# Performance work log

Hardware: AMD Instinct MI355X
Metric: run time of the kernel (lower is better)

Reference implementation:

```python
import jax, jax.numpy as jnp
import numpy as np

B, C, H, W, R = 8, 256, 64, 64, 16


def setup_inputs() -> dict:
    key = jax.random.key(0)
    ks = jax.random.split(key, 14)
    def w(k, shape, fan):
        return (jax.random.normal(k, shape, jnp.float32) / np.sqrt(fan)).astype(jnp.float32)
    return {
        "features_depth": jax.random.normal(ks[0], (B, C, H, W), jnp.float32),
        "features_semseg": jax.random.normal(ks[1], (B, C, H, W), jnp.float32),
        "W0": w(ks[2], (C, 2 * C), 2 * C),          # conv_split0 1x1, [out,in]
        "Wdw": w(ks[3], (C, 1, 3, 3), 9),            # depthwise 3x3, groups=C
        "Wq": w(ks[4], (C, C), C),                   # Linear weights [out,in]
        "Wk": w(ks[5], (C, C), C),
        "Wv": w(ks[6], (C, C), C),
        "Wp": w(ks[7], (C, C), C),
        "bp": jnp.zeros((C,), jnp.float32),
        "Wsplit": w(ks[8], (C, C), C),               # conv_split 1x1
        "se_d_w1": w(ks[9], (C // R, C), C),         # SE squeeze conv1x1 (depth)
        "se_d_w2": w(ks[10], (C, C // R), C // R),
        "se_s_w1": w(ks[11], (C // R, C), C),        # SE squeeze conv1x1 (semseg)
        "se_s_w2": w(ks[12], (C, C // R), C // R),
    }


def _l2norm(a, eps=1e-12):
    n = jnp.linalg.norm(a, axis=-1, keepdims=True)
    return a / jnp.maximum(n, eps)


def _se(x, w1, w2):
    # x: [B,C,H,W]; global avg pool -> 1x1 convs -> sigmoid gate
    p = x.mean(axis=(2, 3))                                  # [B,C]
    h = jax.nn.relu(jnp.einsum('rc,bc->br', w1, p))          # [B,C/R]
    g = jax.nn.sigmoid(jnp.einsum('cr,br->bc', w2, h))       # [B,C]
    return x * g[:, :, None, None]


def reference(features_depth, features_semseg, W0, Wdw, Wq, Wk, Wv, Wp, bp,
              Wsplit, se_d_w1, se_d_w2, se_s_w1, se_s_w2):
    x = jnp.concatenate([features_depth, features_semseg], axis=1)  # [B,2C,H,W]
    x = jnp.einsum('oc,bchw->bohw', W0, x)                          # 1x1 conv
    x = jax.lax.conv_general_dilated(
        x, Wdw, window_strides=(1, 1), padding='SAME',
        dimension_numbers=('NCHW', 'OIHW', 'NCHW'), feature_group_count=C)
    xt = x.transpose(0, 2, 3, 1).reshape(B, H * W, C)               # [B,N,C]
    q = (xt @ Wq.T).transpose(0, 2, 1)                              # [B,C,N]
    k = (xt @ Wk.T).transpose(0, 2, 1)
    v = (xt @ Wv.T).transpose(0, 2, 1)
    q = _l2norm(q)
    k = _l2norm(k)
    attn = jax.nn.softmax(jnp.einsum('bcn,bdn->bcd', k, q), axis=-1)  # [B,C,C]
    y = jnp.einsum('bcd,bdn->bcn', attn, v)                         # [B,C,N]
    y = y.transpose(0, 2, 1)                                        # [B,N,C]
    y = y @ Wp.T + bp                                               # proj
    out_c = y.reshape(B, H, W, C).transpose(0, 3, 1, 2)             # [B,C,H,W]
    out_c = jnp.einsum('oc,bchw->bohw', Wsplit, out_c)              # 1x1 conv
    out_depth = _se(out_c, se_d_w1, se_d_w2) + features_depth
    out_semseg = _se(out_c, se_s_w1, se_s_w2) + features_semseg
    return (out_depth, out_semseg)
```

## Files before the change

kernel.cpp:

```cpp
#include <hip/hip_runtime.h>
#include <cstdint>

#define DEVI __device__ __forceinline__

using fx4 = __attribute__((ext_vector_type(4))) float;
using bf8 = __attribute__((ext_vector_type(8))) __bf16;
using s8v = __attribute__((ext_vector_type(8))) short;
using s4v = __attribute__((ext_vector_type(4))) short;
typedef unsigned short u16;
typedef unsigned int u32;

DEVI float b2f(u16 u) { return __builtin_bit_cast(float, (u32)u << 16); }
DEVI u16 f2b(float f) {
  u32 u = __builtin_bit_cast(u32, f);
  return (u16)((u + 0x7fffu + ((u >> 16) & 1u)) >> 16);
}

#define GLOAD(g, l)                                                          \
  __builtin_amdgcn_global_load_lds(                                          \
      (const __attribute__((address_space(1))) unsigned int*)(g),            \
      (__attribute__((address_space(3))) unsigned int*)(l), 16, 0, 0)

__global__ __launch_bounds__(256) void prep(const float* __restrict__ W0,
                                            const float* __restrict__ Wq,
                                            const float* __restrict__ Wk,
                                            const float* __restrict__ Wv,
                                            u16* __restrict__ w0b,
                                            u16* __restrict__ wqk2,
                                            u16* __restrict__ wvtb) {
  const int i = blockIdx.x * 256 + threadIdx.x;
  if (blockIdx.y == 0) {
    if (i < 131072) w0b[i] = f2b(W0[i]);
  } else if (blockIdx.y == 1) {
    if (i < 524288) {
      const int row = i >> 9, c = i & 511;
      const float* src = (row < 256) ? Wq : Wk;
      wqk2[i] = f2b(src[((row & 255) << 8) + (c & 255)]);
    }
  } else {
    if (i < 65536) {
      const int e = i >> 8, d = i & 255;
      wvtb[i] = f2b(Wv[d * 256 + e]);
    }
  }
}

__global__ __launch_bounds__(256) void wcmul(const float* __restrict__ Wsp,
                                             const float* __restrict__ Wp,
                                             const float* __restrict__ bp,
                                             u16* __restrict__ wcb, float* __restrict__ bc) {
  const int o = blockIdx.x, t = threadIdx.x;
  __shared__ float row[256];
  __shared__ float red[4];
  row[t] = Wsp[o * 256 + t];
  __syncthreads();
  float acc = 0.f;
  for (int c = 0; c < 256; ++c) acc += row[c] * Wp[c * 256 + t];
  wcb[o * 256 + t] = f2b(acc);
  float pb = row[t] * bp[t];
#pragma unroll
  for (int m = 32; m > 0; m >>= 1) pb += __shfl_xor(pb, m);
  if ((t & 63) == 0) red[t >> 6] = pb;
  __syncthreads();
  if (t == 0) bc[o] = red[0] + red[1] + red[2] + red[3];
}

__global__ void pack_cat(const float* __restrict__ fd, const float* __restrict__ fs,
                         u16* __restrict__ out) {
  __shared__ float t[32][33];
  const int b = blockIdx.z;
  const int n0 = blockIdx.x * 32;
  const int g = blockIdx.y;
  const float* src = (g < 8) ? fd : fs;
  const int c0 = (g & 7) * 32;
  const int ccol0 = g * 32;
  const int tx = threadIdx.x;
  const int ty = threadIdx.y;
  const float* sp = src + ((long)b * 256 + c0) * 4096 + n0;
#pragma unroll
  for (int i = 0; i < 4; ++i) {
    int c = ty + i * 8;
    t[c][tx] = sp[(long)c * 4096 + tx];
  }
  __syncthreads();
  u16* op = out + ((long)b * 4096 + n0) * 512 + ccol0;
#pragma unroll
  for (int i = 0; i < 4; ++i) {
    int r = ty + i * 8;
    op[(long)r * 512 + tx] = f2b(t[tx][r]);
  }
}

template <typename OT, int BIAS, bool POOL, int EPI>
__global__ __launch_bounds__(256) void gemm_nt(
    const u16* __restrict__ A, long sA, int lda,
    const u16* __restrict__ B, long sB, int ldb,
    OT* __restrict__ C, long sC, long sCs, int ldc,
    const float* __restrict__ bias, int Keff, int ksplit,
    float* __restrict__ poolpart,
    const float* __restrict__ wqf, const float* __restrict__ wkf,
    float* __restrict__ dpart) {
  __shared__ u16 ldsA[128 * 64];
  __shared__ u16 ldsB[128 * 64];
  const int z = blockIdx.z;
  const int bb = z / ksplit;
  const int ss = z - bb * ksplit;
  const int bm = blockIdx.x * 128;
  const int bn = blockIdx.y * 128;
  const u16* Ab = A + bb * sA + (long)ss * Keff + (long)bm * lda;
  const u16* Bb = B + bb * sB + (long)ss * Keff + (long)bn * ldb;
  const int tid = threadIdx.x;
  const int wid = tid >> 6;
  const int lane = tid & 63;
  const int wm = wid >> 1, wn = wid & 1;
  const int srow = tid >> 3;
  const int slot = tid & 7;

  fx4 acc[4][4] = {};
  for (int kt = 0; kt < Keff; kt += 64) {
#pragma unroll
    for (int i = 0; i < 4; ++i) {
      const int row = i * 32 + srow;
      const int kq = slot ^ (row & 7);
      GLOAD(Ab + (long)row * lda + kt + kq * 8, &ldsA[i * 2048 + wid * 512]);
      GLOAD(Bb + (long)row * ldb + kt + kq * 8, &ldsB[i * 2048 + wid * 512]);
    }
    __syncthreads();
#pragma unroll
    for (int ko = 0; ko < 2; ++ko) {
      bf8 af[4], bfr[4];
      const int kq = ko * 4 + (lane >> 4);
#pragma unroll
      for (int f = 0; f < 4; ++f) {
        const int ar = wm * 64 + f * 16 + (lane & 15);
        af[f] = *(const bf8*)&ldsA[ar * 64 + ((kq ^ (ar & 7)) * 8)];
        const int br = wn * 64 + f * 16 + (lane & 15);
        bfr[f] = *(const bf8*)&ldsB[br * 64 + ((kq ^ (br & 7)) * 8)];
      }
#pragma unroll
      for (int fm = 0; fm < 4; ++fm)
#pragma unroll
        for (int fn = 0; fn < 4; ++fn)
          acc[fm][fn] = __builtin_amdgcn_mfma_f32_16x16x32_bf16(af[fm], bfr[fn], acc[fm][fn], 0, 0, 0);
    }
    __syncthreads();
  }
  if constexpr (EPI == 1) {
    u16* S2b = (u16*)C + bb * sC;
    float dp[4][4];
#pragma unroll
    for (int fm = 0; fm < 4; ++fm)
#pragma unroll
      for (int r = 0; r < 4; ++r) dp[fm][r] = 0.f;
#pragma unroll
    for (int fm = 0; fm < 4; ++fm) {
      const int m0 = bm + wm * 64 + fm * 16 + ((lane >> 4) << 2);
#pragma unroll
      for (int fn = 0; fn < 4; ++fn) {
        const int n0 = bn + wn * 64 + fn * 16 + (lane & 15);
#pragma unroll
        for (int r = 0; r < 4; ++r) {
          const float v = acc[fm][fn][r];
          const int m = m0 + r;
          if (m < 256) {
            const u16 hi = f2b(v);
            S2b[(long)m * 512 + n0] = hi;
            S2b[(long)m * 512 + 256 + n0] = f2b(v - b2f(hi));
          }
          const float* wr = (m < 256) ? (wqf + (long)m * 256) : (wkf + (long)(m - 256) * 256);
          dp[fm][r] += v * wr[n0];
        }
      }
    }
#pragma unroll
    for (int fm = 0; fm < 4; ++fm)
#pragma unroll
      for (int r = 0; r < 4; ++r) {
        float s = dp[fm][r];
        s += __shfl_xor(s, 1); s += __shfl_xor(s, 2);
        s += __shfl_xor(s, 4); s += __shfl_xor(s, 8);
        if ((lane & 15) == 0) {
          const int m = bm + wm * 64 + fm * 16 + ((lane >> 4) << 2) + r;
          dpart[(long)(blockIdx.y * 2 + wn) * 4096 + bb * 512 + m] = s;
        }
      }
    return;
  }
  OT* Cb = C + bb * sC + ss * sCs;
  float pr[4][4];
  if (POOL) {
#pragma unroll
    for (int fm = 0; fm < 4; ++fm)
#pragma unroll
      for (int r = 0; r < 4; ++r) pr[fm][r] = 0.f;
  }
#pragma unroll
  for (int fm = 0; fm < 4; ++fm) {
    const int m0 = bm + wm * 64 + fm * 16 + ((lane >> 4) << 2);
#pragma unroll
    for (int fn = 0; fn < 4; ++fn) {
      const int n0 = bn + wn * 64 + fn * 16 + (lane & 15);
#pragma unroll
      for (int r = 0; r < 4; ++r) {
        float v = acc[fm][fn][r];
        if (BIAS == 2) v += bias[m0 + r];
        if constexpr (sizeof(OT) == 2) Cb[(long)(m0 + r) * ldc + n0] = (OT)f2b(v);
        else Cb[(long)(m0 + r) * ldc + n0] = v;
        if (POOL) pr[fm][r] += v;
      }
    }
  }
  if (POOL) {
#pragma unroll
    for (int fm = 0; fm < 4; ++fm)
#pragma unroll
      for (int r = 0; r < 4; ++r) {
        float s = pr[fm][r];
        s += __shfl_xor(s, 1); s += __shfl_xor(s, 2);
        s += __shfl_xor(s, 4); s += __shfl_xor(s, 8);
        if ((lane & 15) == 0) {
          const int o = bm + wm * 64 + fm * 16 + ((lane >> 4) << 2) + r;
          poolpart[(long)(blockIdx.y * 2 + wn) * 2048 + bb * 256 + o] = s;
        }
      }
  }
}

__global__ __launch_bounds__(256) void dwconv3x3(const u16* __restrict__ x,
                                                 const float* __restrict__ wdw,
                                                 u16* __restrict__ y) {
  __shared__ float w[9][256];
  const int t = threadIdx.x;
  for (int i = t; i < 2304; i += 256) w[i % 9][i / 9] = wdw[i];
  __syncthreads();
  const int nb = blockIdx.x;
  const int b = nb >> 9;
  const int n0 = (nb & 511) << 3;
  const int tn = t >> 5;
  const int tc = (t & 31) << 3;
  const int n = n0 + tn;
  const int hh = n >> 6, ww2 = n & 63;
  const u16* base = x + ((long)b << 20);
  float acc[8] = {0.f, 0.f, 0.f, 0.f, 0.f, 0.f, 0.f, 0.f};
#pragma unroll
  for (int ky = 0; ky < 3; ++ky) {
    const int hy = hh + ky - 1;
    if ((unsigned)hy >= 64u) continue;
#pragma unroll
    for (int kx = 0; kx < 3; ++kx) {
      const int wx = ww2 + kx - 1;
      if ((unsigned)wx >= 64u) continue;
      const s8v v = *(const s8v*)&base[(((hy << 6) + wx) << 8) + tc];
      const int kk = ky * 3 + kx;
      const fx4 wa = *(const fx4*)&w[kk][tc];
      const fx4 wb = *(const fx4*)&w[kk][tc + 4];
#pragma unroll
      for (int j = 0; j < 4; ++j) {
        acc[j] += wa[j] * b2f((u16)v[j]);
        acc[4 + j] += wb[j] * b2f((u16)v[4 + j]);
      }
    }
  }
  s8v o;
#pragma unroll
  for (int j = 0; j < 8; ++j) o[j] = (short)f2b(acc[j]);
  *(s8v*)&y[((long)b << 20) + ((long)n << 8) + tc] = o;
}

__global__ void btrans(const u16* __restrict__ x, u16* __restrict__ y) {
  __shared__ u16 t[32][34];
  const int b = blockIdx.z;
  const int n0 = blockIdx.x * 32;
  const int c0 = blockIdx.y * 32;
  const int tx = threadIdx.x, ty = threadIdx.y;
  const u16* sp = x + (long)b * 1048576 + (long)n0 * 256 + c0;
#pragma unroll
  for (int j = 0; j < 4; ++j) {
    int i = ty + j * 8;
    t[i][tx] = sp[(long)i * 256 + tx];
  }
  __syncthreads();
  u16* op = y + (long)b * 1048576 + (long)c0 * 4096 + n0;
#pragma unroll
  for (int j = 0; j < 4; ++j) {
    int r = ty + j * 8;
    op[(long)r * 4096 + tx] = t[tx][r];
  }
}

__global__ __launch_bounds__(256) void gsplit(const float* __restrict__ part,
                                              u16* __restrict__ G2) {
  const int i4 = (blockIdx.x * 256 + threadIdx.x) * 4;
  fx4 s = {0.f, 0.f, 0.f, 0.f};
#pragma unroll
  for (int ss = 0; ss < 8; ++ss) s += *(const fx4*)(part + (long)ss * 524288 + i4);
  const int b = i4 >> 16, rem = i4 & 65535, e = rem >> 8, c0 = rem & 255;
  u16* d = G2 + (long)b * 131072 + (long)e * 512 + c0;
  s4v hi, lo;
#pragma unroll
  for (int j = 0; j < 4; ++j) {
    u16 h = f2b(s[j]);
    hi[j] = (short)h;
    lo[j] = (short)f2b(s[j] - b2f(h));
  }
  *(s4v*)d = hi;
  *(s4v*)(d + 256) = lo;
}

__global__ __launch_bounds__(256) void softmax_g2(const float* __restrict__ araw,
                                                  const float* __restrict__ dpart,
                                                  u16* __restrict__ out) {
  const int wid = threadIdx.x >> 6, lane = threadIdx.x & 63;
  const int t = threadIdx.x;
  const int b = blockIdx.x >> 6;
  __shared__ float rq[256];
  float dq = dpart[b * 512 + t] + dpart[4096 + b * 512 + t] +
             dpart[8192 + b * 512 + t] + dpart[12288 + b * 512 + t];
  rq[t] = 1.f / fmaxf(sqrtf(fmaxf(dq, 0.f)), 1e-12f);
  __syncthreads();
  const long row = (long)blockIdx.x * 4 + wid;
  const int c = (int)(row & 255);
  const int ki = b * 512 + 256 + c;
  float dk = dpart[ki] + dpart[4096 + ki] + dpart[8192 + ki] + dpart[12288 + ki];
  const float rk = 1.f / fmaxf(sqrtf(fmaxf(dk, 0.f)), 1e-12f);
  fx4 v = ((const fx4*)(araw + row * 256))[lane];
  v[0] *= rk * rq[lane * 4];     v[1] *= rk * rq[lane * 4 + 1];
  v[2] *= rk * rq[lane * 4 + 2]; v[3] *= rk * rq[lane * 4 + 3];
  float m = fmaxf(fmaxf(v[0], v[1]), fmaxf(v[2], v[3]));
#pragma unroll
  for (int o = 32; o > 0; o >>= 1) m = fmaxf(m, __shfl_xor(m, o));
  float e0 = __expf(v[0] - m), e1 = __expf(v[1] - m);
  float e2 = __expf(v[2] - m), e3 = __expf(v[3] - m);
  float s4 = e0 + e1 + e2 + e3;
#pragma unroll
  for (int o = 32; o > 0; o >>= 1) s4 += __shfl_xor(s4, o);
  const float inv = 1.f / s4;
  u16* op = out + row * 256 + lane * 4;
  op[0] = f2b(e0 * inv); op[1] = f2b(e1 * inv);
  op[2] = f2b(e2 * inv); op[3] = f2b(e3 * inv);
}

__global__ __launch_bounds__(256) void se_gates(const float* __restrict__ poolpart,
                                                const float* __restrict__ w1d, const float* __restrict__ w2d,
                                                const float* __restrict__ w1s, const float* __restrict__ w2s,
                                                float* __restrict__ gd, float* __restrict__ gs) {
  const int b = blockIdx.x;
  const int t = threadIdx.x;
  __shared__ float p[256], hd[16], hs[16];
  float s = 0.f;
#pragma unroll 8
  for (int sl = 0; sl < 64; ++sl) s += poolpart[(long)sl * 2048 + b * 256 + t];
  p[t] = s * (1.f / 4096.f);
  __syncthreads();
  if (t < 16) {
    float ad = 0.f, as2 = 0.f;
    for (int j = 0; j < 256; ++j) {
      ad += w1d[t * 256 + j] * p[j];
      as2 += w1s[t * 256 + j] * p[j];
    }
    hd[t] = fmaxf(ad, 0.f);
    hs[t] = fmaxf(as2, 0.f);
  }
  __syncthreads();
  float ad = 0.f, as2 = 0.f;
#pragma unroll
  for (int r = 0; r < 16; ++r) {
    ad += w2d[t * 16 + r] * hd[r];
    as2 += w2s[t * 16 + r] * hs[r];
  }
  gd[b * 256 + t] = 1.f / (1.f + __expf(-ad));
  gs[b * 256 + t] = 1.f / (1.f + __expf(-as2));
}

__global__ __launch_bounds__(256) void fuse_out2(const u16* __restrict__ oc,
                                                 const u16* __restrict__ cat,
                                                 const float* __restrict__ gd,
                                                 const float* __restrict__ gs,
                                                 float* __restrict__ od,
                                                 float* __restrict__ os) {
  __shared__ u16 td[32][68];
  __shared__ u16 ts2[32][68];
  const int b = blockIdx.z;
  const int c0 = blockIdx.y * 32;
  const int n0 = blockIdx.x * 64;
  const int t = threadIdx.x;
  {
    const int n = t >> 2, cj = (t & 3) * 8;
    const u16* cb = cat + ((long)b * 4096 + n0 + n) * 512 + c0 + cj;
    const s8v vd = *(const s8v*)cb;
    const s8v vs = *(const s8v*)(cb + 256);
#pragma unroll
    for (int j = 0; j < 8; ++j) {
      td[cj + j][n] = (u16)vd[j];
      ts2[cj + j][n] = (u16)vs[j];
    }
  }
  __syncthreads();
  const int c = t >> 3, no = (t & 7) * 8;
  const long obase = ((long)b * 256 + c0 + c) * 4096 + n0 + no;
  const float gdv = gd[b * 256 + c0 + c];
  const float gsv = gs[b * 256 + c0 + c];
  const s8v o8 = *(const s8v*)&oc[obase];
  fx4 r0, r1, q0, q1;
#pragma unroll
  for (int j = 0; j < 4; ++j) {
    const float vl = b2f((u16)o8[j]);
    const float vh = b2f((u16)o8[4 + j]);
    r0[j] = vl * gdv + b2f(td[c][no + j]);
    r1[j] = vh * gdv + b2f(td[c][no + 4 + j]);
    q0[j] = vl * gsv + b2f(ts2[c][no + j]);
    q1[j] = vh * gsv + b2f(ts2[c][no + 4 + j]);
  }
  *(fx4*)(od + obase) = r0; *(fx4*)(od + obase + 4) = r1;
  *(fx4*)(os + obase) = q0; *(fx4*)(os + obase + 4) = q1;
}

extern "C" void kernel_launch(void* const* d_in, const int* in_sizes, int n_in,
                              void* d_out, int out_size, void* d_ws, size_t ws_size,
                              hipStream_t stream) {
  const float* fd  = (const float*)d_in[0];
  const float* fs  = (const float*)d_in[1];
  const float* W0  = (const float*)d_in[2];
  const float* Wdw = (const float*)d_in[3];
  const float* Wq  = (const float*)d_in[4];
  const float* Wk  = (const float*)d_in[5];
  const float* Wv  = (const float*)d_in[6];
  const float* Wp  = (const float*)d_in[7];
  const float* bp  = (const float*)d_in[8];
  const float* Wsp = (const float*)d_in[9];
  const float* w1d = (const float*)d_in[10];
  const float* w2d = (const float*)d_in[11];
  const float* w1s = (const float*)d_in[12];
  const float* w2s = (const float*)d_in[13];

  char* ws = (char*)d_ws;
  u16* catb   = (u16*)(ws + 0);
  u16* x0b    = (u16*)(ws + 33554432);
  u16* outcb  = x0b;
  u16* xtb    = (u16*)(ws + 50331648);
  u16* xtT    = (u16*)(ws + 67108864);
  float* part = (float*)(ws + 83886080);
  u16* G2     = (u16*)(ws + 100663296);
  u16* S2     = (u16*)(ws + 102760448);
  float* araw = (float*)(ws + 104857600);
  u16* attnb  = (u16*)(ws + 106954752);
  u16* m1t    = (u16*)(ws + 108003328);
  u16* wfin   = (u16*)(ws + 109051904);
  u16* w0b    = (u16*)(ws + 110100480);
  u16* wqk2   = (u16*)(ws + 110362624);
  u16* wvtb   = (u16*)(ws + 110886912);
  u16* wcb    = (u16*)(ws + 111017984);
  float* bcb  = (float*)(ws + 111149056);
  float* dpart = (float*)(ws + 111150080);
  float* poolpart = (float*)(ws + 111215616);
  float* gdp  = (float*)(ws + 111739904);
  float* gsp  = (float*)(ws + 111748096);
  float* od  = (float*)d_out;
  float* osg = od + 8388608;

  prep<<<dim3(2048, 3), 256, 0, stream>>>(W0, Wq, Wk, Wv, w0b, wqk2, wvtb);
  wcmul<<<256, 256, 0, stream>>>(Wsp, Wp, bp, wcb, bcb);
  pack_cat<<<dim3(128, 16, 8), dim3(32, 8), 0, stream>>>(fd, fs, catb);
  gemm_nt<u16, 0, false, 0><<<dim3(32, 2, 8), 256, 0, stream>>>(
      catb, 2097152, 512, w0b, 0, 512, x0b, 1048576, 0, 256, nullptr, 512, 1,
      nullptr, nullptr, nullptr, nullptr);
  dwconv3x3<<<4096, 256, 0, stream>>>(x0b, Wdw, xtb);
  btrans<<<dim3(128, 8, 8), dim3(32, 8), 0, stream>>>(xtb, xtT);
  gemm_nt<float, 0, false, 0><<<dim3(2, 2, 64), 256, 0, stream>>>(
      xtT, 1048576, 4096, xtT, 1048576, 4096,
      part, 65536, 524288, 256, nullptr, 512, 8, nullptr, nullptr, nullptr, nullptr);
  gsplit<<<512, 256, 0, stream>>>(part, G2);
  gemm_nt<u16, 0, false, 1><<<dim3(4, 2, 8), 256, 0, stream>>>(
      wqk2, 0, 512, G2, 131072, 512, S2, 131072, 0, 512, nullptr, 512, 1,
      nullptr, Wq, Wk, dpart);
  gemm_nt<float, 0, false, 0><<<dim3(2, 2, 8), 256, 0, stream>>>(
      wqk2 + 131072, 0, 512, S2, 131072, 512, araw, 65536, 0, 256, nullptr, 512, 1,
      nullptr, nullptr, nullptr, nullptr);
  softmax_g2<<<512, 256, 0, stream>>>(araw, dpart, attnb);
  gemm_nt<u16, 0, false, 0><<<dim3(2, 2, 8), 256, 0, stream>>>(
      wvtb, 0, 256, attnb, 65536, 256, m1t, 65536, 0, 256, nullptr, 256, 1,
      nullptr, nullptr, nullptr, nullptr);
  gemm_nt<u16, 0, false, 0><<<dim3(2, 2, 8), 256, 0, stream>>>(
      wcb, 0, 256, m1t, 65536, 256, wfin, 65536, 0, 256, nullptr, 256, 1,
      nullptr, nullptr, nullptr, nullptr);
  gemm_nt<u16, 2, true, 0><<<dim3(2, 32, 8), 256, 0, stream>>>(
      wfin, 65536, 256, xtb, 1048576, 256, outcb, 1048576, 0, 4096, bcb, 256, 1,
      poolpart, nullptr, nullptr, nullptr);
  se_gates<<<8, 256, 0, stream>>>(poolpart, w1d, w2d, w1s, w2s, gdp, gsp);
  fuse_out2<<<dim3(64, 8, 8), 256, 0, stream>>>(outcb, catb, gdp, gsp, od, osg);
}
```

Before: 182.8 us.

## Fuse input packing into conv0 GEMM, fold split-K reduction into downstream GEMM

Replaces the pack_cat transpose-to-bf16 kernel and the first 1x1 GEMM with a single conv0f kernel. It reads fp32 features directly, converts and transposes them through LDS, and runs the MFMA GEMM. The Gram split-K partials are now written as hi/lo bf16 pairs straight from the GEMM epilogue, and the gsplit reduction is removed. The next GEMM sums the 8 partials implicitly through a K=4096 contraction against a replicated Wq/Wk matrix. The wcmul weight prep is merged into prep, and fuse_out reads the original fp32 features instead of the bf16 concat buffer. This cuts launches and intermediate traffic, at the cost of an 8x larger K in the QK GEMM and a conv0 kernel with no load pipelining.

```diff
diff --git a/kernel.cpp b/kernel.cpp
--- a/kernel.cpp
+++ b/kernel.cpp
@@ -25,69 +25,125 @@
                                             const float* __restrict__ Wq,
                                             const float* __restrict__ Wk,
                                             const float* __restrict__ Wv,
+                                            const float* __restrict__ Wsp,
+                                            const float* __restrict__ Wp,
+                                            const float* __restrict__ bp,
                                             u16* __restrict__ w0b,
-                                            u16* __restrict__ wqk2,
-                                            u16* __restrict__ wvtb) {
-  const int i = blockIdx.x * 256 + threadIdx.x;
-  if (blockIdx.y == 0) {
+                                            u16* __restrict__ wqk8,
+                                            u16* __restrict__ wvtb,
+                                            u16* __restrict__ wcb,
+                                            float* __restrict__ bcb) {
+  __shared__ float row[256];
+  __shared__ float red[4];
+  const int y = blockIdx.y;
+  const int t = threadIdx.x;
+  if (y == 0) {
+    const int i = blockIdx.x * 256 + t;
     if (i < 131072) w0b[i] = f2b(W0[i]);
-  } else if (blockIdx.y == 1) {
-    if (i < 524288) {
-      const int row = i >> 9, c = i & 511;
-      const float* src = (row < 256) ? Wq : Wk;
-      wqk2[i] = f2b(src[((row & 255) << 8) + (c & 255)]);
-    }
-  } else {
+  } else if (y == 1) {
+    const int i = blockIdx.x * 256 + t;
+    const int r = i >> 10;
+    const int q = (i & 1023) * 4;
+    const int yy = q & 255;
+    const float* src = (r < 256) ? (Wq + r * 256) : (Wk + (r - 256) * 256);
+    s4v o;
+#pragma unroll
+    for (int j = 0; j < 4; ++j) o[j] = (short)f2b(src[yy + j]);
+    *(s4v*)&wqk8[(long)r * 4096 + q] = o;
+  } else if (y == 2) {
+    const int i = blockIdx.x * 256 + t;
     if (i < 65536) {
       const int e = i >> 8, d = i & 255;
       wvtb[i] = f2b(Wv[d * 256 + e]);
     }
-  }
-}
-
-__global__ __launch_bounds__(256) void wcmul(const float* __restrict__ Wsp,
-                                             const float* __restrict__ Wp,
-                                             const float* __restrict__ bp,
-                                             u16* __restrict__ wcb, float* __restrict__ bc) {
-  const int o = blockIdx.x, t = threadIdx.x;
-  __shared__ float row[256];
-  __shared__ float red[4];
-  row[t] = Wsp[o * 256 + t];
-  __syncthreads();
-  float acc = 0.f;
-  for (int c = 0; c < 256; ++c) acc += row[c] * Wp[c * 256 + t];
-  wcb[o * 256 + t] = f2b(acc);
-  float pb = row[t] * bp[t];
-#pragma unroll
-  for (int m = 32; m > 0; m >>= 1) pb += __shfl_xor(pb, m);
-  if ((t & 63) == 0) red[t >> 6] = pb;
-  __syncthreads();
-  if (t == 0) bc[o] = red[0] + red[1] + red[2] + red[3];
-}
-
-__global__ void pack_cat(const float* __restrict__ fd, const float* __restrict__ fs,
-                         u16* __restrict__ out) {
-  __shared__ float t[32][33];
-  const int b = blockIdx.z;
-  const int n0 = blockIdx.x * 32;
-  const int g = blockIdx.y;
-  const float* src = (g < 8) ? fd : fs;
-  const int c0 = (g & 7) * 32;
-  const int ccol0 = g * 32;
-  const int tx = threadIdx.x;
-  const int ty = threadIdx.y;
-  const float* sp = src + ((long)b * 256 + c0) * 4096 + n0;
-#pragma unroll
-  for (int i = 0; i < 4; ++i) {
-    int c = ty + i * 8;
-    t[c][tx] = sp[(long)c * 4096 + tx];
-  }
-  __syncthreads();
-  u16* op = out + ((long)b * 4096 + n0) * 512 + ccol0;
-#pragma unroll
-  for (int i = 0; i < 4; ++i) {
-    int r = ty + i * 8;
-    op[(long)r * 512 + tx] = f2b(t[tx][r]);
+  } else {
+    if (blockIdx.x >= 256) return;
+    const int o = blockIdx.x;
+    row[t] = Wsp[o * 256 + t];
+    __syncthreads();
+    float acc = 0.f;
+    for (int c = 0; c < 256; ++c) acc += row[c] * Wp[c * 256 + t];
+    wcb[o * 256 + t] = f2b(acc);
+    float pb = row[t] * bp[t];
+#pragma unroll
+    for (int m = 32; m > 0; m >>= 1) pb += __shfl_xor(pb, m);
+    if ((t & 63) == 0) red[t >> 6] = pb;
+    __syncthreads();
+    if (t == 0) bcb[o] = red[0] + red[1] + red[2] + red[3];
+  }
+}
+
+__global__ __launch_bounds__(512) void conv0f(const float* __restrict__ fd,
+                                              const float* __restrict__ fs,
+                                              const u16* __restrict__ w0b,
+                                              u16* __restrict__ x0) {
+  __shared__ u16 tmp[64 * 132];
+  __shared__ u16 ldsA[128 * 64];
+  __shared__ u16 ldsB[256 * 64];
+  const int b = blockIdx.y;
+  const int bm = blockIdx.x * 128;
+  const int t = threadIdx.x;
+  const int wid = t >> 6, lane = t & 63;
+  const int wm = wid >> 2, wn = wid & 3;
+  fx4 acc[4][4] = {};
+  for (int kt = 0; kt < 512; kt += 64) {
+#pragma unroll
+    for (int i = 0; i < 4; ++i) {
+      const int r = i * 64 + (t >> 3);
+      const int kq = (t & 7) ^ (r & 7);
+      GLOAD(w0b + (long)r * 512 + kt + kq * 8, &ldsB[i * 4096 + wid * 512]);
+    }
+    const float* src = ((kt < 256) ? fd : fs) + ((long)b * 256 + (kt & 255)) * 4096L + bm;
+#pragma unroll
+    for (int p = 0; p < 4; ++p) {
+      const int c = (t >> 5) + p * 16;
+      const int n4 = (t & 31) * 4;
+      const fx4 v = *(const fx4*)&src[(long)c * 4096 + n4];
+      s4v pk;
+#pragma unroll
+      for (int j = 0; j < 4; ++j) pk[j] = (short)f2b(v[j]);
+      *(s4v*)&tmp[c * 132 + n4] = pk;
+    }
+    __syncthreads();
+#pragma unroll
+    for (int pass = 0; pass < 2; ++pass) {
+      const int n = t & 127;
+      const int g = (t >> 7) + pass * 4;
+      s8v pk;
+#pragma unroll
+      for (int j = 0; j < 8; ++j) pk[j] = (short)tmp[(g * 8 + j) * 132 + n];
+      *(s8v*)&ldsA[n * 64 + ((g ^ (n & 7)) * 8)] = pk;
+    }
+    __syncthreads();
+#pragma unroll
+    for (int ko = 0; ko < 2; ++ko) {
+      bf8 af[4], bfr[4];
+      const int kq = ko * 4 + (lane >> 4);
+#pragma unroll
+      for (int f = 0; f < 4; ++f) {
+        const int ar = wm * 64 + f * 16 + (lane & 15);
+        af[f] = *(const bf8*)&ldsA[ar * 64 + ((kq ^ (ar & 7)) * 8)];
+        const int br = wn * 64 + f * 16 + (lane & 15);
+        bfr[f] = *(const bf8*)&ldsB[br * 64 + ((kq ^ (br & 7)) * 8)];
+      }
+#pragma unroll
+      for (int fm = 0; fm < 4; ++fm)
+#pragma unroll
+        for (int fn = 0; fn < 4; ++fn)
+          acc[fm][fn] = __builtin_amdgcn_mfma_f32_16x16x32_bf16(af[fm], bfr[fn], acc[fm][fn], 0, 0, 0);
+    }
+    __syncthreads();
+  }
+#pragma unroll
+  for (int fm = 0; fm < 4; ++fm) {
+    const int m0 = wm * 64 + fm * 16 + ((lane >> 4) << 2);
+#pragma unroll
+    for (int fn = 0; fn < 4; ++fn) {
+      const int o = wn * 64 + fn * 16 + (lane & 15);
+#pragma unroll
+      for (int r = 0; r < 4; ++r)
+        x0[((long)b << 20) + (long)(bm + m0 + r) * 256 + o] = f2b(acc[fm][fn][r]);
+    }
   }
 }
 
@@ -145,6 +201,26 @@
     }
     __syncthreads();
   }
+  if constexpr (EPI == 3) {
+    u16* Pb = (u16*)C + bb * sC;
+#pragma unroll
+    for (int fm = 0; fm < 4; ++fm) {
+      const int m0 = bm + wm * 64 + fm * 16 + ((lane >> 4) << 2);
+#pragma unroll
+      for (int fn = 0; fn < 4; ++fn) {
+        const int n0 = bn + wn * 64 + fn * 16 + (lane & 15);
+#pragma unroll
+        for (int r = 0; r < 4; ++r) {
+          const float v = acc[fm][fn][r];
+          const u16 hi = f2b(v);
+          const long base = (long)(m0 + r) * 4096 + ss * 512 + n0;
+          Pb[base] = hi;
+          Pb[base + 256] = f2b(v - b2f(hi));
+        }
+      }
+    }
+    return;
+  }
   if constexpr (EPI == 1) {
     u16* S2b = (u16*)C + bb * sC;
     float dp[4][4];
@@ -286,25 +362,6 @@
     int r = ty + j * 8;
     op[(long)r * 4096 + tx] = t[tx][r];
   }
-}
-
-__global__ __launch_bounds__(256) void gsplit(const float* __restrict__ part,
-                                              u16* __restrict__ G2) {
-  const int i4 = (blockIdx.x * 256 + threadIdx.x) * 4;
-  fx4 s = {0.f, 0.f, 0.f, 0.f};
-#pragma unroll
-  for (int ss = 0; ss < 8; ++ss) s += *(const fx4*)(part + (long)ss * 524288 + i4);
-  const int b = i4 >> 16, rem = i4 & 65535, e = rem >> 8, c0 = rem & 255;
-  u16* d = G2 + (long)b * 131072 + (long)e * 512 + c0;
-  s4v hi, lo;
-#pragma unroll
-  for (int j = 0; j < 4; ++j) {
-    u16 h = f2b(s[j]);
-    hi[j] = (short)h;
-    lo[j] = (short)f2b(s[j] - b2f(h));
-  }
-  *(s4v*)d = hi;
-  *(s4v*)(d + 256) = lo;
 }
 
 __global__ __launch_bounds__(256) void softmax_g2(const float* __restrict__ araw,
@@ -372,47 +429,26 @@
   gs[b * 256 + t] = 1.f / (1.f + __expf(-as2));
 }
 
-__global__ __launch_bounds__(256) void fuse_out2(const u16* __restrict__ oc,
-                                                 const u16* __restrict__ cat,
-                                                 const float* __restrict__ gd,
-                                                 const float* __restrict__ gs,
-                                                 float* __restrict__ od,
-                                                 float* __restrict__ os) {
-  __shared__ u16 td[32][68];
-  __shared__ u16 ts2[32][68];
-  const int b = blockIdx.z;
-  const int c0 = blockIdx.y * 32;
-  const int n0 = blockIdx.x * 64;
-  const int t = threadIdx.x;
-  {
-    const int n = t >> 2, cj = (t & 3) * 8;
-    const u16* cb = cat + ((long)b * 4096 + n0 + n) * 512 + c0 + cj;
-    const s8v vd = *(const s8v*)cb;
-    const s8v vs = *(const s8v*)(cb + 256);
-#pragma unroll
-    for (int j = 0; j < 8; ++j) {
-      td[cj + j][n] = (u16)vd[j];
-      ts2[cj + j][n] = (u16)vs[j];
-    }
-  }
-  __syncthreads();
-  const int c = t >> 3, no = (t & 7) * 8;
-  const long obase = ((long)b * 256 + c0 + c) * 4096 + n0 + no;
-  const float gdv = gd[b * 256 + c0 + c];
-  const float gsv = gs[b * 256 + c0 + c];
-  const s8v o8 = *(const s8v*)&oc[obase];
-  fx4 r0, r1, q0, q1;
+__global__ __launch_bounds__(256) void fuse_out(const u16* __restrict__ oc,
+                                                const float* __restrict__ gd, const float* __restrict__ gs,
+                                                const float* __restrict__ fd, const float* __restrict__ fs,
+                                                float* __restrict__ od, float* __restrict__ os) {
+  const long i = ((long)blockIdx.x * 256 + threadIdx.x) * 8;
+  const long bc = i >> 12;
+  const float gdv = gd[bc], gsv = gs[bc];
+  const s8v c8 = *(const s8v*)&oc[i];
+  const fx4 a0 = *(const fx4*)(fd + i), a1 = *(const fx4*)(fd + i + 4);
+  const fx4 s0 = *(const fx4*)(fs + i), s1 = *(const fx4*)(fs + i + 4);
+  fx4 d0, d1, e0, e1;
 #pragma unroll
   for (int j = 0; j < 4; ++j) {
-    const float vl = b2f((u16)o8[j]);
-    const float vh = b2f((u16)o8[4 + j]);
-    r0[j] = vl * gdv + b2f(td[c][no + j]);
-    r1[j] = vh * gdv + b2f(td[c][no + 4 + j]);
-    q0[j] = vl * gsv + b2f(ts2[c][no + j]);
-    q1[j] = vh * gsv + b2f(ts2[c][no + 4 + j]);
-  }
-  *(fx4*)(od + obase) = r0; *(fx4*)(od + obase + 4) = r1;
-  *(fx4*)(os + obase) = q0; *(fx4*)(os + obase + 4) = q1;
+    const float cl = b2f((u16)c8[j]);
+    const float ch = b2f((u16)c8[4 + j]);
+    d0[j] = cl * gdv + a0[j]; d1[j] = ch * gdv + a1[j];
+    e0[j] = cl * gsv + s0[j]; e1[j] = ch * gsv + s1[j];
+  }
+  *(fx4*)(od + i) = d0; *(fx4*)(od + i + 4) = d1;
+  *(fx4*)(os + i) = e0; *(fx4*)(os + i + 4) = e1;
 }
 
 extern "C" void kernel_launch(void* const* d_in, const int* in_sizes, int n_in,
@@ -434,48 +470,42 @@
   const float* w2s = (const float*)d_in[13];
 
   char* ws = (char*)d_ws;
-  u16* catb   = (u16*)(ws + 0);
-  u16* x0b    = (u16*)(ws + 33554432);
+  u16* x0b    = (u16*)(ws + 0);
   u16* outcb  = x0b;
-  u16* xtb    = (u16*)(ws + 50331648);
-  u16* xtT    = (u16*)(ws + 67108864);
-  float* part = (float*)(ws + 83886080);
-  u16* G2     = (u16*)(ws + 100663296);
-  u16* S2     = (u16*)(ws + 102760448);
-  float* araw = (float*)(ws + 104857600);
-  u16* attnb  = (u16*)(ws + 106954752);
-  u16* m1t    = (u16*)(ws + 108003328);
-  u16* wfin   = (u16*)(ws + 109051904);
-  u16* w0b    = (u16*)(ws + 110100480);
-  u16* wqk2   = (u16*)(ws + 110362624);
-  u16* wvtb   = (u16*)(ws + 110886912);
-  u16* wcb    = (u16*)(ws + 111017984);
-  float* bcb  = (float*)(ws + 111149056);
-  float* dpart = (float*)(ws + 111150080);
-  float* poolpart = (float*)(ws + 111215616);
-  float* gdp  = (float*)(ws + 111739904);
-  float* gsp  = (float*)(ws + 111748096);
+  u16* xtb    = (u16*)(ws + 16777216);
+  u16* xtT    = (u16*)(ws + 33554432);
+  u16* part2  = (u16*)(ws + 50331648);
+  u16* S2     = (u16*)(ws + 67108864);
+  float* araw = (float*)(ws + 69206016);
+  u16* attnb  = (u16*)(ws + 71303168);
+  u16* m1t    = (u16*)(ws + 72351744);
+  u16* wfin   = (u16*)(ws + 73400320);
+  u16* w0b    = (u16*)(ws + 74448896);
+  u16* wqk8   = (u16*)(ws + 74711040);
+  u16* wvtb   = (u16*)(ws + 78905344);
+  u16* wcb    = (u16*)(ws + 79036416);
+  float* bcb  = (float*)(ws + 79167488);
+  float* dpart = (float*)(ws + 79168512);
+  float* poolpart = (float*)(ws + 79234048);
+  float* gdp  = (float*)(ws + 79758336);
+  float* gsp  = (float*)(ws + 79766528);
   float* od  = (float*)d_out;
   float* osg = od + 8388608;
 
-  prep<<<dim3(2048, 3), 256, 0, stream>>>(W0, Wq, Wk, Wv, w0b, wqk2, wvtb);
-  wcmul<<<256, 256, 0, stream>>>(Wsp, Wp, bp, wcb, bcb);
-  pack_cat<<<dim3(128, 16, 8), dim3(32, 8), 0, stream>>>(fd, fs, catb);
-  gemm_nt<u16, 0, false, 0><<<dim3(32, 2, 8), 256, 0, stream>>>(
-      catb, 2097152, 512, w0b, 0, 512, x0b, 1048576, 0, 256, nullptr, 512, 1,
-      nullptr, nullptr, nullptr, nullptr);
+  prep<<<dim3(2048, 4), 256, 0, stream>>>(W0, Wq, Wk, Wv, Wsp, Wp, bp,
+                                          w0b, wqk8, wvtb, wcb, bcb);
+  conv0f<<<dim3(32, 8), 512, 0, stream>>>(fd, fs, w0b, x0b);
   dwconv3x3<<<4096, 256, 0, stream>>>(x0b, Wdw, xtb);
   btrans<<<dim3(128, 8, 8), dim3(32, 8), 0, stream>>>(xtb, xtT);
-  gemm_nt<float, 0, false, 0><<<dim3(2, 2, 64), 256, 0, stream>>>(
+  gemm_nt<u16, 0, false, 3><<<dim3(2, 2, 64), 256, 0, stream>>>(
       xtT, 1048576, 4096, xtT, 1048576, 4096,
-      part, 65536, 524288, 256, nullptr, 512, 8, nullptr, nullptr, nullptr, nullptr);
-  gsplit<<<512, 256, 0, stream>>>(part, G2);
+      part2, 1048576, 0, 4096, nullptr, 512, 8, nullptr, nullptr, nullptr, nullptr);
   gemm_nt<u16, 0, false, 1><<<dim3(4, 2, 8), 256, 0, stream>>>(
-      wqk2, 0, 512, G2, 131072, 512, S2, 131072, 0, 512, nullptr, 512, 1,
+      wqk8, 0, 4096, part2, 1048576, 4096, S2, 131072, 0, 512, nullptr, 4096, 1,
       nullptr, Wq, Wk, dpart);
   gemm_nt<float, 0, false, 0><<<dim3(2, 2, 8), 256, 0, stream>>>(
-      wqk2 + 131072, 0, 512, S2, 131072, 512, araw, 65536, 0, 256, nullptr, 512, 1,
-      nullptr, nullptr, nullptr, nullptr);
+      wqk8 + (long)256 * 4096, 0, 4096, S2, 131072, 512, araw, 65536, 0, 256,
+      nullptr, 512, 1, nullptr, nullptr, nullptr, nullptr);
   softmax_g2<<<512, 256, 0, stream>>>(araw, dpart, attnb);
   gemm_nt<u16, 0, false, 0><<<dim3(2, 2, 8), 256, 0, stream>>>(
       wvtb, 0, 256, attnb, 65536, 256, m1t, 65536, 0, 256, nullptr, 256, 1,
@@ -487,5 +517,5 @@
       wfin, 65536, 256, xtb, 1048576, 256, outcb, 1048576, 0, 4096, bcb, 256, 1,
       poolpart, nullptr, nullptr, nullptr);
   se_gates<<<8, 256, 0, stream>>>(poolpart, w1d, w2d, w1s, w2s, gdp, gsp);
-  fuse_out2<<<dim3(64, 8, 8), 256, 0, stream>>>(outcb, catb, gdp, gsp, od, osg);
-}
+  fuse_out<<<4096, 256, 0, stream>>>(outcb, gdp, gsp, fd, fs, od, osg);
+}
```

Result: slower. 229.8 us (+25.7%).
